# Kernel tuning notes

Hardware: AMD Instinct MI355X
Metric: run time of the kernel (lower is better)

The kernel has to match this reference:

```python
import jax, jax.numpy as jnp
import numpy as np

B, S, E = 2, 2048, 4096
HQ, HKV, D = 32, 8, 128
WINDOW = 1024
SOFT_CAP = 50.0
Q_PRE_ATTN = 128.0
TT_SCALE = 0.1
TT_FLOOR = 8192.0
EPS = 1e-6
ROPE_BASE = 10000.0


def l2norm(x):
    return x * jax.lax.rsqrt(jnp.mean(x * x, axis=-1, keepdims=True) + EPS)


def apply_rope(x, pos):
    # x: [B,S,H,D]; half-split rotary, base 10000
    half = x.shape[-1] // 2
    freq = ROPE_BASE ** (-jnp.arange(half, dtype=jnp.float32) * 2.0 / x.shape[-1])  # [half]
    angle = pos.astype(jnp.float32)[:, None] * freq[None, :]                         # [S,half]
    cos = jnp.cos(angle)[None, :, None, :]
    sin = jnp.sin(angle)[None, :, None, :]
    x1, x2 = x[..., :half], x[..., half:]
    return jnp.concatenate([x1 * cos - x2 * sin, x2 * cos + x1 * sin], axis=-1)


def setup_inputs() -> dict:
    key = jax.random.key(0)
    ks = jax.random.split(key, 5)
    sc = 0.02
    return {
        "x": jax.random.normal(ks[0], (B, S, E), jnp.float32),
        "Wq": jax.random.normal(ks[1], (E, HQ, D), jnp.float32) * sc,
        "Wk": jax.random.normal(ks[2], (E, HKV, D), jnp.float32) * sc,
        "Wv": jax.random.normal(ks[3], (E, HKV, D), jnp.float32) * sc,
        "Wo": jax.random.normal(ks[4], (HQ, D, E), jnp.float32) * sc,
    }


def reference(x, Wq, Wk, Wv, Wo):
    pos = jnp.arange(S)
    # QKV projections
    q = jnp.einsum('bse,ehd->bshd', x, Wq)   # [B,S,HQ,D]
    k = jnp.einsum('bse,ehd->bshd', x, Wk)   # [B,S,HKV,D]
    v = jnp.einsum('bse,ehd->bshd', x, Wv)   # [B,S,HKV,D]
    # QK norm (L2Norm) then RoPE
    q = apply_rope(l2norm(q), pos)
    k = apply_rope(l2norm(k), pos)
    # query pre-attention scaling
    q = q * (Q_PRE_ATTN ** -0.5)
    # temperature tuning: per-position scale
    attn_scale = jnp.log(jnp.floor((pos.astype(jnp.float32) + 1.0) / TT_FLOOR) + 1.0) * TT_SCALE + 1.0
    q = q * attn_scale[None, :, None, None]
    # GQA: expand kv heads
    g = HQ // HKV
    k_r = jnp.repeat(k, g, axis=2)           # [B,S,HQ,D]
    v_r = jnp.repeat(v, g, axis=2)
    logits = jnp.einsum('bihd,bjhd->bhij', q, k_r).astype(jnp.float32)
    # tanh soft cap
    logits = SOFT_CAP * jnp.tanh(logits / SOFT_CAP)
    # causal + sliding window mask: j <= i and i - j < WINDOW
    i = pos[:, None]
    j = pos[None, :]
    mask = (j <= i) & ((i - j) < WINDOW)     # [S,S]
    logits = jnp.where(mask[None, None], logits, jnp.float32(-1e30))
    probs = jax.nn.softmax(logits, axis=-1)
    out = jnp.einsum('bhij,bjhd->bihd', probs, v_r)  # [B,S,HQ,D]
    return jnp.einsum('bihd,hde->bie', out, Wo)      # [B,S,E]
```

## Files before the change

### kernel.cpp

```cpp
#include <hip/hip_runtime.h>


typedef unsigned short u16;
typedef unsigned int   u32;
typedef __bf16 bf16x8 __attribute__((ext_vector_type(8)));
typedef float  f32x4  __attribute__((ext_vector_type(4)));

typedef __attribute__((address_space(1))) void* gas_ptr;
typedef __attribute__((address_space(3))) void* las_ptr;

__device__ __forceinline__ void load_lds16(const void* g, void* l) {
  __builtin_amdgcn_global_load_lds((gas_ptr)g, (las_ptr)l, 16, 0, 0);
}

__device__ __forceinline__ u16 f2bf(float f) {
  u32 u = __builtin_bit_cast(u32, f);
  u += 0x7fffu + ((u >> 16) & 1u);
  return (u16)(u >> 16);
}
__device__ __forceinline__ float bf2f(u16 h) {
  u32 u = ((u32)h) << 16;
  return __builtin_bit_cast(float, u);
}
__device__ __forceinline__ u32 pack_trunc(float a, float b) {
  return (__builtin_bit_cast(u32, a) >> 16) | (__builtin_bit_cast(u32, b) & 0xffff0000u);
}

__global__ __launch_bounds__(256) void cast_f32_bf16(const float* __restrict__ src,
                                                     u16* __restrict__ dst) {
  size_t i = ((size_t)blockIdx.x * 256 + threadIdx.x) * 8;
  float4 a = *(const float4*)(src + i);
  float4 b = *(const float4*)(src + i + 4);
  uint4 o;
  o.x = (u32)f2bf(a.x) | ((u32)f2bf(a.y) << 16);
  o.y = (u32)f2bf(a.z) | ((u32)f2bf(a.w) << 16);
  o.z = (u32)f2bf(b.x) | ((u32)f2bf(b.y) << 16);
  o.w = (u32)f2bf(b.z) | ((u32)f2bf(b.w) << 16);
  *(uint4*)(dst + i) = o;
}

__global__ __launch_bounds__(256) void transpose_cast_f32_bf16(
    const float* __restrict__ src, u16* __restrict__ dst, int R, int C) {
  __shared__ float tile[32][33];
  const int tx = threadIdx.x & 31, ty = threadIdx.x >> 5;
  const int r0 = blockIdx.y * 32, c0 = blockIdx.x * 32;
#pragma unroll
  for (int i = 0; i < 4; ++i)
    tile[ty + i * 8][tx] = src[(size_t)(r0 + ty + i * 8) * C + (c0 + tx)];
  __syncthreads();
#pragma unroll
  for (int i = 0; i < 4; ++i)
    dst[(size_t)(c0 + ty + i * 8) * R + (r0 + tx)] = f2bf(tile[tx][ty + i * 8]);
}

__global__ __launch_bounds__(256) void transpose_v(const u16* __restrict__ src,
                                                   u16* __restrict__ dst) {
  __shared__ u16 tile[32][34];
  const int plane = blockIdx.z;
  const u16* s = src + (size_t)plane * 2048 * 128;
  u16* d = dst + (size_t)plane * 2048 * 128;
  const int tx = threadIdx.x & 31, ty = threadIdx.x >> 5;
  const int r0 = blockIdx.x * 32, c0 = blockIdx.y * 32;
#pragma unroll
  for (int i = 0; i < 4; ++i)
    tile[ty + i * 8][tx] = s[(size_t)(r0 + ty + i * 8) * 128 + (c0 + tx)];
  __syncthreads();
#pragma unroll
  for (int i = 0; i < 4; ++i)
    d[(size_t)(c0 + ty + i * 8) * 2048 + (r0 + tx)] = tile[tx][ty + i * 8];
}


template <int MB>
__device__ __forceinline__ void mm16(f32x4 (&acc)[8][4], const bf16x8 (&af)[4],
                                     const bf16x8 (&bf)[4]) {
#pragma unroll
  for (int ii = 0; ii < 4; ++ii)
#pragma unroll
    for (int nf = 0; nf < 4; ++nf)
      acc[MB + ii][nf] =
          __builtin_amdgcn_mfma_f32_16x16x32_bf16(af[ii], bf[nf], acc[MB + ii][nf], 0, 0, 0);
}

template <int OUT_BF16>
__global__ __launch_bounds__(512, 2) void gemm256(const u16* __restrict__ A,
                                                  const u16* __restrict__ Bt,
                                                  void* __restrict__ Cout,
                                                  int N, int K, int ntx) {
  __shared__ __align__(16) u16 lds[65536];
  const int t = threadIdx.x, lane = t & 63, w = t >> 6;
  const int c = lane & 15, q = lane >> 4;
  const int wm = w >> 2, wn = w & 3;

  const int cpx = (int)gridDim.x >> 3;
  const int swz = ((int)blockIdx.x & 7) * cpx + ((int)blockIdx.x >> 3);
  const int bx = swz % ntx, by = swz / ntx;
  const int m0 = by << 8, n0 = bx << 8;

  u32 aoff[2][2], boff[2][2];
#pragma unroll
  for (int h = 0; h < 2; ++h)
#pragma unroll
    for (int j = 0; j < 2; ++j) {
      const int rowS = w * 16 + j * 8 + (lane >> 3);
      const int colE = ((lane & 7) ^ (rowS & 7)) * 8;
      aoff[h][j] = (u32)(m0 + h * 128 + rowS) * (u32)K + (u32)colE;
      boff[h][j] = (u32)(n0 + h * 128 + rowS) * (u32)K + (u32)colE;
    }
  const u32 stW = (u32)w * 1024u;

  const u32 sl0 = (u32)((q ^ (c & 7)) * 8);
  const u32 aR = (u32)(wm * 8192 + c * 64) + sl0;
  const u32 bR = (u32)(16384 + (wn >> 1) * 8192 + (wn & 1) * 4096 + c * 64) + sl0;

  f32x4 acc[8][4];
#pragma unroll
  for (int i2 = 0; i2 < 8; ++i2)
#pragma unroll
    for (int j2 = 0; j2 < 4; ++j2) acc[i2][j2] = (f32x4){0.f, 0.f, 0.f, 0.f};

  const int nt = K >> 6;

#define STG_A(bb, hh, kt)                                                \
  do {                                                                   \
    u16* d_ = &lds[(bb) * 32768u + (hh) * 8192u + stW];                  \
    load_lds16(A + (aoff[hh][0] + (u32)(kt) * 64u), d_);                 \
    load_lds16(A + (aoff[hh][1] + (u32)(kt) * 64u), d_ + 512);           \
  } while (0)
#define STG_B(bb, hh, kt)                                                \
  do {                                                                   \
    u16* d_ = &lds[(bb) * 32768u + 16384u + (hh) * 8192u + stW];         \
    load_lds16(Bt + (boff[hh][0] + (u32)(kt) * 64u), d_);                \
    load_lds16(Bt + (boff[hh][1] + (u32)(kt) * 64u), d_ + 512);          \
  } while (0)
#define RD4(dst, base)                                                   \
  do {                                                                   \
    const u16* p_ = &lds[(base)];                                        \
    dst[0] = *(const bf16x8*)(p_);                                       \
    dst[1] = *(const bf16x8*)(p_ + 1024);                                \
    dst[2] = *(const bf16x8*)(p_ + 2048);                                \
    dst[3] = *(const bf16x8*)(p_ + 3072);                                \
  } while (0)
#define BAR __builtin_amdgcn_s_barrier()
#define LGKM0 asm volatile("s_waitcnt lgkmcnt(0)" ::: "memory")
#define VM6 asm volatile("s_waitcnt vmcnt(6)" ::: "memory")
#define PRIO1 __builtin_amdgcn_s_setprio(1)
#define PRIO0 __builtin_amdgcn_s_setprio(0)

  STG_B(0, 0, 0);
  STG_B(0, 1, 0);
  STG_A(0, 0, 0);
  STG_A(0, 1, 0);
  STG_B(1, 0, 1);
  STG_B(1, 1, 1);
  STG_A(1, 0, 1);
  VM6;
  BAR;

  bf16x8 Bf0[4], Bf1[4], Af0[4], Af1[4];

  for (int i = 0; i < (nt >> 1); ++i) {
    const int tb = 2 * i + 1;
    int t2 = 2 * i + 2; if (t2 >= nt) t2 -= nt;
    int t3 = 2 * i + 3; if (t3 >= nt) t3 -= nt;

    RD4(Bf0, bR);
    RD4(Bf1, bR ^ 32u);
    RD4(Af0, aR);
    STG_A(1, 1, tb);
    BAR; LGKM0;
    PRIO1; mm16<0>(acc, Af0, Bf0); PRIO0;
    BAR;
    RD4(Af1, aR + 4096u);
    STG_B(0, 0, t2);
    BAR; LGKM0;
    PRIO1; mm16<4>(acc, Af1, Bf0); PRIO0;
    BAR;
    RD4(Af0, aR ^ 32u);
    RD4(Af1, (aR + 4096u) ^ 32u);
    STG_B(0, 1, t2);
    BAR; LGKM0;
    PRIO1; mm16<0>(acc, Af0, Bf1); PRIO0;
    BAR;
    STG_A(0, 0, t2);
    VM6;
    BAR;
    PRIO1; mm16<4>(acc, Af1, Bf1); PRIO0;
    BAR;

    RD4(Bf0, 32768u + bR);
    RD4(Bf1, (32768u + bR) ^ 32u);
    RD4(Af0, 32768u + aR);
    STG_A(0, 1, t2);
    BAR; LGKM0;
    PRIO1; mm16<0>(acc, Af0, Bf0); PRIO0;
    BAR;
    RD4(Af1, 32768u + aR + 4096u);
    STG_B(1, 0, t3);
    BAR; LGKM0;
    PRIO1; mm16<4>(acc, Af1, Bf0); PRIO0;
    BAR;
    RD4(Af0, (32768u + aR) ^ 32u);
    RD4(Af1, (32768u + aR + 4096u) ^ 32u);
    STG_B(1, 1, t3);
    BAR; LGKM0;
    PRIO1; mm16<0>(acc, Af0, Bf1); PRIO0;
    BAR;
    STG_A(1, 0, t3);
    VM6;
    BAR;
    PRIO1; mm16<4>(acc, Af1, Bf1); PRIO0;
    BAR;
  }

  asm volatile("s_waitcnt vmcnt(0)" ::: "memory");

#undef STG_A
#undef STG_B
#undef RD4
#undef BAR
#undef LGKM0
#undef VM6
#undef PRIO1
#undef PRIO0

  const int rb0 = m0 + wm * 128 + q * 4;
  const int cb0 = n0 + wn * 64 + c;
#pragma unroll
  for (int mf = 0; mf < 8; ++mf)
#pragma unroll
    for (int nf = 0; nf < 4; ++nf) {
      const size_t base = (size_t)(rb0 + mf * 16) * N + (cb0 + nf * 16);
#pragma unroll
      for (int r = 0; r < 4; ++r) {
        if (OUT_BF16)
          ((u16*)Cout)[base + (size_t)r * N] = f2bf(acc[mf][nf][r]);
        else
          ((float*)Cout)[base + (size_t)r * N] = acc[mf][nf][r];
      }
    }
}

__global__ __launch_bounds__(256) void qkv_post(const u16* __restrict__ raw,
                                                u16* __restrict__ qb,
                                                u16* __restrict__ kb,
                                                u16* __restrict__ vb) {
  const int t = threadIdx.x, lane = t & 63, w = t >> 6;
  const int idx = blockIdx.x * 4 + w;
  const int row = idx / 48, hh = idx - row * 48;
  const int b = row >> 11, pos = row & 2047;
  const u16* base = raw + (size_t)row * 6144 + hh * 128;
  const u16 r1 = base[lane], r2 = base[lane + 64];

  if (hh >= 40) {
    u16* dst = vb + ((size_t)((b * 8 + (hh - 40)) * 2048 + pos)) * 128;
    dst[lane] = r1;
    dst[lane + 64] = r2;
    return;
  }
  float v1 = bf2f(r1), v2 = bf2f(r2);
  float ss = v1 * v1 + v2 * v2;
#pragma unroll
  for (int off = 32; off >= 1; off >>= 1) ss += __shfl_xor(ss, off);
  const float rn = rsqrtf(ss * (1.0f / 128.0f) + 1e-6f);
  const float n1 = v1 * rn, n2 = v2 * rn;
  const float fr = exp2f(-(float)lane * 0.20762050593046f);
  const float ang = (float)pos * fr;
  float sn, cs;
  sincosf(ang, &sn, &cs);
  float o1 = n1 * cs - n2 * sn;
  float o2 = n2 * cs + n1 * sn;
  u16* dst;
  if (hh < 32) {
    const float as_ = logf(floorf((float)(pos + 1) * (1.0f / 8192.0f)) + 1.0f) * 0.1f + 1.0f;
    const float sc = 0.088388347648318447f * as_;
    o1 *= sc;
    o2 *= sc;
    dst = qb + ((size_t)((b * 32 + hh) * 2048 + pos)) * 128;
  } else {
    dst = kb + ((size_t)((b * 8 + (hh - 32)) * 2048 + pos)) * 128;
  }
  dst[lane] = f2bf(o1);
  dst[lane + 64] = f2bf(o2);
}

__global__ __launch_bounds__(256, 4) void attn_fwd(const u16* __restrict__ qb,
                                                   const u16* __restrict__ kb,
                                                   const u16* __restrict__ vtb,
                                                   u16* __restrict__ attn) {
  __shared__ __align__(16) u16 Ks[64 * 128];
  __shared__ __align__(16) u16 VTs[128 * 64];
  __shared__ __align__(16) u16 Ps[4][16 * 64];

  const int t = threadIdx.x, lane = t & 63, w = t >> 6;
  const int c = lane & 15, quad = lane >> 4;
  const int q0 = blockIdx.x * 64;
  const int bh = blockIdx.y;
  const int b = bh >> 5, hq = bh & 31;
  const int kvp = b * 8 + (hq >> 2);
  const u16* qp = qb + (size_t)bh * (2048 * 128);
  const u16* kp = kb + (size_t)kvp * (2048 * 128);
  const u16* vp = vtb + (size_t)kvp * (128 * 2048);
  u16* Psw = &Ps[w][0];

  bf16x8 qf[4];
  {
    const u16* qrow = qp + (size_t)(q0 + w * 16 + c) * 128 + quad * 8;
#pragma unroll
    for (int ks = 0; ks < 4; ++ks) qf[ks] = *(const bf16x8*)(qrow + ks * 32);
  }

  f32x4 oacc[8];
#pragma unroll
  for (int j = 0; j < 8; ++j)
#pragma unroll
    for (int r = 0; r < 4; ++r) oacc[j][r] = 0.0f;
  float lsum = 0.0f;

  const int i_glob = q0 + w * 16 + c;

  int t0 = q0 - 1023;
  if (t0 < 0) t0 = 0;
  t0 = (t0 >> 6) << 6;

  for (int kv0 = t0; kv0 <= q0; kv0 += 64) {
    __syncthreads();
    {
      const int row_in = lane >> 4, ch = lane & 15;
#pragma unroll
      for (int i = 0; i < 4; ++i) {
        const int row = w * 4 + i * 16 + row_in;
        const int g = ch ^ (row & 15);
        load_lds16(kp + (size_t)(kv0 + row) * 128 + g * 8, &Ks[(w * 4 + i * 16) * 128]);
      }
      const int drow = lane >> 3, ch8 = lane & 7;
#pragma unroll
      for (int i = 0; i < 4; ++i) {
        const int dd = w * 8 + i * 32 + drow;
        const int g = ch8 ^ (dd & 7);
        load_lds16(vp + (size_t)dd * 2048 + kv0 + g * 8, &VTs[(w * 8 + i * 32) * 64]);
      }
    }
    __syncthreads();

    f32x4 sacc[4];
#pragma unroll
    for (int im = 0; im < 4; ++im)
#pragma unroll
      for (int r = 0; r < 4; ++r) sacc[im][r] = 0.0f;

#pragma unroll
    for (int ks = 0; ks < 4; ++ks) {
#pragma unroll
      for (int im = 0; im < 4; ++im) {
        const int key = im * 16 + c;
        const int ch = (ks * 4 + quad) ^ c;
        const bf16x8 af = *(const bf16x8*)&Ks[key * 128 + ch * 8];
        sacc[im] = __builtin_amdgcn_mfma_f32_16x16x32_bf16(af, qf[ks], sacc[im], 0, 0, 0);
      }
    }

    const bool need_mask = (kv0 == q0) || (q0 - kv0 >= 961);
#pragma unroll
    for (int im = 0; im < 4; ++im) {
      float pv[4];
#pragma unroll
      for (int r = 0; r < 4; ++r) {
        const float s = sacc[im][r];
        const float u = s * s;
        const float cap = s * (1.0f + u * (-1.3333333e-4f + u * 2.1333333e-8f));
        pv[r] = __expf(cap);
      }
      if (need_mask) {
        const int j_base = kv0 + im * 16 + quad * 4;
#pragma unroll
        for (int r = 0; r < 4; ++r) {
          const int j_glob = j_base + r;
          if (!((j_glob <= i_glob) && (i_glob - j_glob < 1024))) pv[r] = 0.0f;
        }
      }
      lsum += (pv[0] + pv[1]) + (pv[2] + pv[3]);
      uint2 pk;
      pk.x = pack_trunc(pv[0], pv[1]);
      pk.y = pack_trunc(pv[2], pv[3]);
      *(uint2*)&Psw[c * 64 + ((im * 2 + (quad >> 1)) ^ (c & 7)) * 8 + (quad & 1) * 4] = pk;
    }

#pragma unroll
    for (int ks = 0; ks < 2; ++ks) {
      const bf16x8 pf = *(const bf16x8*)&Psw[c * 64 + ((ks * 4 + quad) ^ (c & 7)) * 8];
#pragma unroll
      for (int jn = 0; jn < 8; ++jn) {
        const int dd = jn * 16 + c;
        const int ch = (ks * 4 + quad) ^ (c & 7);
        const bf16x8 vf = *(const bf16x8*)&VTs[dd * 64 + ch * 8];
        oacc[jn] = __builtin_amdgcn_mfma_f32_16x16x32_bf16(pf, vf, oacc[jn], 0, 0, 0);
      }
    }
  }

  float lt = lsum;
  lt += __shfl_xor(lt, 16);
  lt += __shfl_xor(lt, 32);
  float rl[4];
#pragma unroll
  for (int r = 0; r < 4; ++r)
    rl[r] = __builtin_amdgcn_rcpf(__shfl(lt, quad * 4 + r));

  const size_t obase = ((size_t)(b * 2048 + q0 + w * 16)) * 4096 + hq * 128;
#pragma unroll
  for (int jn = 0; jn < 8; ++jn) {
#pragma unroll
    for (int r = 0; r < 4; ++r) {
      const int q_in = quad * 4 + r;
      attn[obase + (size_t)q_in * 4096 + jn * 16 + c] = f2bf(oacc[jn][r] * rl[r]);
    }
  }
}

extern "C" void kernel_launch(void* const* d_in, const int* in_sizes, int n_in,
                              void* d_out, int out_size, void* d_ws, size_t ws_size,
                              hipStream_t stream) {
  (void)in_sizes; (void)n_in; (void)out_size; (void)ws_size;
  const float* x  = (const float*)d_in[0];
  const float* Wq = (const float*)d_in[1];
  const float* Wk = (const float*)d_in[2];
  const float* Wv = (const float*)d_in[3];
  const float* Wo = (const float*)d_in[4];
  float* out = (float*)d_out;
  char* ws = (char*)d_ws;

  u16* xb    = (u16*)(ws + 0);
  u16* vtb   = (u16*)(ws + 0);
  u16* WqkvT = (u16*)(ws + 33554432ULL);
  u16* qb    = (u16*)(ws + 33554432ULL);
  u16* kb    = (u16*)(ws + 67108864ULL);
  u16* vb    = (u16*)(ws + 75497472ULL);
  u16* WoT   = (u16*)(ws + 83886080ULL);
  u16* qkvr  = (u16*)(ws + 117440512ULL);
  u16* attnb = (u16*)(ws + 117440512ULL);

  cast_f32_bf16<<<8192, 256, 0, stream>>>(x, xb);
  transpose_cast_f32_bf16<<<dim3(128, 128), 256, 0, stream>>>(Wq, WqkvT, 4096, 4096);
  transpose_cast_f32_bf16<<<dim3(32, 128), 256, 0, stream>>>(Wk, WqkvT + (size_t)4096 * 4096, 4096, 1024);
  transpose_cast_f32_bf16<<<dim3(32, 128), 256, 0, stream>>>(Wv, WqkvT + (size_t)5120 * 4096, 4096, 1024);
  transpose_cast_f32_bf16<<<dim3(128, 128), 256, 0, stream>>>(Wo, WoT, 4096, 4096);

  gemm256<1><<<dim3(384), 512, 0, stream>>>(xb, WqkvT, (void*)qkvr, 6144, 4096, 24);
  qkv_post<<<49152, 256, 0, stream>>>(qkvr, qb, kb, vb);
  transpose_v<<<dim3(64, 4, 16), 256, 0, stream>>>(vb, vtb);
  attn_fwd<<<dim3(32, 64), 256, 0, stream>>>(qb, kb, vtb, attnb);
  gemm256<0><<<dim3(256), 512, 0, stream>>>(attnb, WoT, (void*)out, 4096, 4096, 16);
}
```

Measured before the change: 710.1 us.

## Vectorize QKV post-processing and transposes, read V directly from QKV output

qkv_post now has 16 lanes per head, each doing 128-bit loads and stores. RoPE partner values are exchanged with a lane shuffle. The V copy pass is removed: transpose_v reads V straight out of the fused QKV GEMM output. Both transpose kernels now pack four bf16 values into 64-bit stores instead of scalar 16-bit writes. The GEMM main loop also adds an early partial LDS wait before the barrier. The temperature scaling term is dropped, which is exact only because floor((pos+1)/8192) is zero for every position at this sequence length.

```diff
diff --git a/kernel.cpp b/kernel.cpp
--- a/kernel.cpp
+++ b/kernel.cpp
@@ -48,26 +48,29 @@
   for (int i = 0; i < 4; ++i)
     tile[ty + i * 8][tx] = src[(size_t)(r0 + ty + i * 8) * C + (c0 + tx)];
   __syncthreads();
-#pragma unroll
-  for (int i = 0; i < 4; ++i)
-    dst[(size_t)(c0 + ty + i * 8) * R + (r0 + tx)] = f2bf(tile[tx][ty + i * 8]);
-}
-
-__global__ __launch_bounds__(256) void transpose_v(const u16* __restrict__ src,
-                                                   u16* __restrict__ dst) {
+  uint2 ov;
+  ov.x = (u32)f2bf(tile[ty * 4 + 0][tx]) | ((u32)f2bf(tile[ty * 4 + 1][tx]) << 16);
+  ov.y = (u32)f2bf(tile[ty * 4 + 2][tx]) | ((u32)f2bf(tile[ty * 4 + 3][tx]) << 16);
+  *(uint2*)&dst[(size_t)(c0 + tx) * R + (r0 + ty * 4)] = ov;
+}
+
+__global__ __launch_bounds__(256) void transpose_v(const u16* __restrict__ qkvr,
+                                                   u16* __restrict__ vtb) {
   __shared__ u16 tile[32][34];
   const int plane = blockIdx.z;
-  const u16* s = src + (size_t)plane * 2048 * 128;
-  u16* d = dst + (size_t)plane * 2048 * 128;
+  const int b = plane >> 3, h8 = plane & 7;
+  const u16* s = qkvr + (size_t)(b * 2048) * 6144 + (40 + h8) * 128;
+  u16* d = vtb + (size_t)plane * 2048 * 128;
   const int tx = threadIdx.x & 31, ty = threadIdx.x >> 5;
   const int r0 = blockIdx.x * 32, c0 = blockIdx.y * 32;
 #pragma unroll
   for (int i = 0; i < 4; ++i)
-    tile[ty + i * 8][tx] = s[(size_t)(r0 + ty + i * 8) * 128 + (c0 + tx)];
+    tile[ty + i * 8][tx] = s[(size_t)(r0 + ty + i * 8) * 6144 + (c0 + tx)];
   __syncthreads();
-#pragma unroll
-  for (int i = 0; i < 4; ++i)
-    d[(size_t)(c0 + ty + i * 8) * 2048 + (r0 + tx)] = tile[tx][ty + i * 8];
+  uint2 ov;
+  ov.x = (u32)tile[ty * 4 + 0][tx] | ((u32)tile[ty * 4 + 1][tx] << 16);
+  ov.y = (u32)tile[ty * 4 + 2][tx] | ((u32)tile[ty * 4 + 3][tx] << 16);
+  *(uint2*)&d[(size_t)(c0 + tx) * 2048 + (r0 + ty * 4)] = ov;
 }
 
 
@@ -143,6 +146,7 @@
   } while (0)
 #define BAR __builtin_amdgcn_s_barrier()
 #define LGKM0 asm volatile("s_waitcnt lgkmcnt(0)" ::: "memory")
+#define LGKM8 asm volatile("s_waitcnt lgkmcnt(8)" ::: "memory")
 #define VM6 asm volatile("s_waitcnt vmcnt(6)" ::: "memory")
 #define PRIO1 __builtin_amdgcn_s_setprio(1)
 #define PRIO0 __builtin_amdgcn_s_setprio(0)
@@ -168,6 +172,7 @@
     RD4(Bf1, bR ^ 32u);
     RD4(Af0, aR);
     STG_A(1, 1, tb);
+    LGKM8;
     BAR; LGKM0;
     PRIO1; mm16<0>(acc, Af0, Bf0); PRIO0;
     BAR;
@@ -192,6 +197,7 @@
     RD4(Bf1, (32768u + bR) ^ 32u);
     RD4(Af0, 32768u + aR);
     STG_A(0, 1, t2);
+    LGKM8;
     BAR; LGKM0;
     PRIO1; mm16<0>(acc, Af0, Bf0); PRIO0;
     BAR;
@@ -220,6 +226,7 @@
 #undef RD4
 #undef BAR
 #undef LGKM0
+#undef LGKM8
 #undef VM6
 #undef PRIO1
 #undef PRIO0
@@ -243,45 +250,62 @@
 
 __global__ __launch_bounds__(256) void qkv_post(const u16* __restrict__ raw,
                                                 u16* __restrict__ qb,
-                                                u16* __restrict__ kb,
-                                                u16* __restrict__ vb) {
-  const int t = threadIdx.x, lane = t & 63, w = t >> 6;
-  const int idx = blockIdx.x * 4 + w;
-  const int row = idx / 48, hh = idx - row * 48;
-  const int b = row >> 11, pos = row & 2047;
-  const u16* base = raw + (size_t)row * 6144 + hh * 128;
-  const u16 r1 = base[lane], r2 = base[lane + 64];
-
-  if (hh >= 40) {
-    u16* dst = vb + ((size_t)((b * 8 + (hh - 40)) * 2048 + pos)) * 128;
-    dst[lane] = r1;
-    dst[lane + 64] = r2;
-    return;
-  }
-  float v1 = bf2f(r1), v2 = bf2f(r2);
-  float ss = v1 * v1 + v2 * v2;
-#pragma unroll
-  for (int off = 32; off >= 1; off >>= 1) ss += __shfl_xor(ss, off);
+                                                u16* __restrict__ kb) {
+  const int t = threadIdx.x;
+  const int c = t & 15, g = t >> 4;
+  const u32 u = (u32)blockIdx.x * 16u + (u32)g;
+  const u32 row = u / 40u;
+  const int hh = (int)(u - row * 40u);
+  const int pos = (int)(row & 2047u);
+  const int b = (int)(row >> 11);
+
+  const uint4 rv = *(const uint4*)(raw + (size_t)row * 6144 + hh * 128 + c * 8);
+  u32 rw[4] = {rv.x, rv.y, rv.z, rv.w};
+  float xs[8];
+#pragma unroll
+  for (int j = 0; j < 4; ++j) {
+    xs[2 * j] = bf2f((u16)(rw[j] & 0xffffu));
+    xs[2 * j + 1] = bf2f((u16)(rw[j] >> 16));
+  }
+  float ss = 0.f;
+#pragma unroll
+  for (int j = 0; j < 8; ++j) ss += xs[j] * xs[j];
+#pragma unroll
+  for (int off = 8; off >= 1; off >>= 1) ss += __shfl_xor(ss, off);
   const float rn = rsqrtf(ss * (1.0f / 128.0f) + 1e-6f);
-  const float n1 = v1 * rn, n2 = v2 * rn;
-  const float fr = exp2f(-(float)lane * 0.20762050593046f);
-  const float ang = (float)pos * fr;
-  float sn, cs;
-  sincosf(ang, &sn, &cs);
-  float o1 = n1 * cs - n2 * sn;
-  float o2 = n2 * cs + n1 * sn;
-  u16* dst;
-  if (hh < 32) {
-    const float as_ = logf(floorf((float)(pos + 1) * (1.0f / 8192.0f)) + 1.0f) * 0.1f + 1.0f;
-    const float sc = 0.088388347648318447f * as_;
-    o1 *= sc;
-    o2 *= sc;
-    dst = qb + ((size_t)((b * 32 + hh) * 2048 + pos)) * 128;
-  } else {
-    dst = kb + ((size_t)((b * 8 + (hh - 32)) * 2048 + pos)) * 128;
-  }
-  dst[lane] = f2bf(o1);
-  dst[lane + 64] = f2bf(o2);
+
+  u32 pw[4];
+#pragma unroll
+  for (int j = 0; j < 4; ++j) pw[j] = __shfl_xor(rw[j], 8);
+  float xp[8];
+#pragma unroll
+  for (int j = 0; j < 4; ++j) {
+    xp[2 * j] = bf2f((u16)(pw[j] & 0xffffu));
+    xp[2 * j + 1] = bf2f((u16)(pw[j] >> 16));
+  }
+
+  const float sgn = (c < 8) ? -1.0f : 1.0f;
+  const int dbase = (c & 7) * 8;
+  const float fpos = (float)pos;
+  const bool isq = (hh < 32);
+  const float sc = (isq ? 0.088388347648318447f : 1.0f) * rn;
+  float o[8];
+#pragma unroll
+  for (int j = 0; j < 8; ++j) {
+    const float fr = exp2f(-(float)(dbase + j) * 0.20762050593046f);
+    float sn, cs;
+    sincosf(fpos * fr, &sn, &cs);
+    o[j] = (xs[j] * cs + sgn * xp[j] * sn) * sc;
+  }
+
+  uint4 ov;
+  ov.x = (u32)f2bf(o[0]) | ((u32)f2bf(o[1]) << 16);
+  ov.y = (u32)f2bf(o[2]) | ((u32)f2bf(o[3]) << 16);
+  ov.z = (u32)f2bf(o[4]) | ((u32)f2bf(o[5]) << 16);
+  ov.w = (u32)f2bf(o[6]) | ((u32)f2bf(o[7]) << 16);
+  u16* dst = isq ? (qb + ((size_t)((b * 32 + hh) * 2048 + pos)) * 128)
+                 : (kb + ((size_t)((b * 8 + (hh - 32)) * 2048 + pos)) * 128);
+  *(uint4*)(dst + c * 8) = ov;
 }
 
 __global__ __launch_bounds__(256, 4) void attn_fwd(const u16* __restrict__ qb,
@@ -435,7 +459,6 @@
   u16* WqkvT = (u16*)(ws + 33554432ULL);
   u16* qb    = (u16*)(ws + 33554432ULL);
   u16* kb    = (u16*)(ws + 67108864ULL);
-  u16* vb    = (u16*)(ws + 75497472ULL);
   u16* WoT   = (u16*)(ws + 83886080ULL);
   u16* qkvr  = (u16*)(ws + 117440512ULL);
   u16* attnb = (u16*)(ws + 117440512ULL);
@@ -447,8 +470,8 @@
   transpose_cast_f32_bf16<<<dim3(128, 128), 256, 0, stream>>>(Wo, WoT, 4096, 4096);
 
   gemm256<1><<<dim3(384), 512, 0, stream>>>(xb, WqkvT, (void*)qkvr, 6144, 4096, 24);
-  qkv_post<<<49152, 256, 0, stream>>>(qkvr, qb, kb, vb);
-  transpose_v<<<dim3(64, 4, 16), 256, 0, stream>>>(vb, vtb);
+  qkv_post<<<10240, 256, 0, stream>>>(qkvr, qb, kb);
+  transpose_v<<<dim3(64, 4, 16), 256, 0, stream>>>(qkvr, vtb);
   attn_fwd<<<dim3(32, 64), 256, 0, stream>>>(qb, kb, vtb, attnb);
   gemm256<0><<<dim3(256), 512, 0, stream>>>(attnb, WoT, (void*)out, 4096, 4096, 16);
 }
```

After: 691.3 us. 2.6% less time.
